# Kernel optimization log

Hardware: AMD Instinct MI355X
Metric: run time of the kernel (lower is better)

## Reference

```python
import jax, jax.numpy as jnp
import numpy as np

B, S, D, V, MAXLEN, K = 1, 2048, 768, 32000, 2048, 3
EPS = 1.1920929e-07  # torch.finfo(float32).eps, nn.RMSNorm default


def _linear_init(key, fan_in, fan_out):
    kw, kb = jax.random.split(key)
    bound = 1.0 / np.sqrt(fan_in)
    w = jax.random.uniform(kw, (fan_in, fan_out), minval=-bound, maxval=bound, dtype=jnp.float32)
    b = jax.random.uniform(kb, (fan_out,), minval=-bound, maxval=bound, dtype=jnp.float32)
    return w, b


def setup_inputs() -> dict:
    key = jax.random.key(0)
    ks = jax.random.split(key, 12)
    x = jax.random.randint(ks[0], (B, S), 0, V, dtype=jnp.int64)
    embedding = jax.random.normal(ks[1], (V, D), dtype=jnp.float32)
    pos_emb = jax.random.normal(ks[2], (MAXLEN, D), dtype=jnp.float32)
    # conv1d weight (out, in, k) torch layout
    bound = 1.0 / np.sqrt(D * K)
    conv_w = jax.random.uniform(ks[3], (D, D, K), minval=-bound, maxval=bound, dtype=jnp.float32)
    conv_b = jax.random.uniform(ks[4], (D,), minval=-bound, maxval=bound, dtype=jnp.float32)
    wg1, bg1 = _linear_init(ks[5], D, D)
    wmv, bmv = _linear_init(ks[6], 2 * D, D)
    wmg, bmg = _linear_init(ks[7], 2 * D, D)
    wrg, brg = _linear_init(ks[8], 2 * D, D)
    whw, bhw = _linear_init(ks[9], D, D)
    rms_w = jnp.ones((D,), dtype=jnp.float32)
    wpred, bpred = _linear_init(ks[10], D, V)
    return dict(x=x, embedding=embedding, pos_emb=pos_emb, conv_w=conv_w, conv_b=conv_b,
                wg1=wg1, bg1=bg1, wmv=wmv, bmv=bmv, wmg=wmg, bmg=bmg,
                wrg=wrg, brg=brg, whw=whw, bhw=bhw, rms_w=rms_w, wpred=wpred, bpred=bpred)


def _rmsnorm(x, w):
    ms = jnp.mean(jnp.square(x), axis=-1, keepdims=True)
    return x * jax.lax.rsqrt(ms + EPS) * w


def _causal_conv(x, conv_w, conv_b):
    # x: [B,S,D] -> left-pad by K-1, conv1d, back to [B,S,D]
    xc = jnp.transpose(x, (0, 2, 1))  # [B,D,S]
    y = jax.lax.conv_general_dilated(
        xc, conv_w, window_strides=(1,), padding=[(K - 1, 0)],
        dimension_numbers=('NCH', 'OIH', 'NCH'))
    y = y + conv_b[None, :, None]
    return jnp.transpose(y, (0, 2, 1))


def reference(x, embedding, pos_emb, conv_w, conv_b, wg1, bg1, wmv, bmv, wmg, bmg,
              wrg, brg, whw, bhw, rms_w, wpred, bpred):
    seq_len = x.shape[1]
    h = embedding[x] + pos_emb[:seq_len][None, :, :]
    h = _causal_conv(h, conv_w, conv_b)
    nodes = h * jax.nn.sigmoid(h @ wg1 + bg1)
    # Hillis-Steele log-depth causal scan
    curr = nodes
    step = 1
    while step < seq_len:
        left = curr[:, :-step, :]
        right = curr[:, step:, :]
        comb = jnp.concatenate([left, right], axis=-1)
        val = comb @ wmv + bmv
        gate = jax.nn.sigmoid(comb @ wmg + bmg)
        merged = _rmsnorm(val * gate, rms_w)
        hg = jax.nn.sigmoid(right @ whw + bhw)
        merged = hg * merged + (1.0 - hg) * right
        rg = jax.nn.sigmoid(comb @ wrg + brg)
        merged = rg * merged + (1.0 - rg) * (left + right) * 0.5
        curr = curr.at[:, step:, :].set(merged)
        step *= 2
    return curr @ wpred + bpred
```

## Files before the change

kernel.cpp:

```cpp
#include <hip/hip_runtime.h>
#include <hip/hip_bf16.h>

typedef __attribute__((ext_vector_type(8))) short short8;
typedef __attribute__((ext_vector_type(4))) float floatx4;
typedef __hip_bfloat16 bf16_t;

#define DD 768

__device__ __forceinline__ float sigmoid_f(float x) { return 1.f / (1.f + __expf(-x)); }

__device__ __forceinline__ void gl2lds16(const void* g, void* l) {
  __builtin_amdgcn_global_load_lds((const __attribute__((address_space(1))) void*)g,
                                   (__attribute__((address_space(3))) void*)l, 16, 0, 0);
}

__global__ __launch_bounds__(512, 2) void gemm256(
    const bf16_t* __restrict__ A, int lda, int M,
    const bf16_t* __restrict__ Wt, int Kdim,
    int nRowT, int nColT,
    const float* __restrict__ bias,
    float* __restrict__ out, int N)
{
  __shared__ __attribute__((aligned(16))) unsigned char lds[163840];
  const int tid = threadIdx.x;
  const int wave = tid >> 6, lane = tid & 63;
  const int l15 = lane & 15, kq = lane >> 4;
  const int wm = wave >> 2, wn = wave & 3;

  const int nwg = gridDim.x;
  const int q8 = nwg >> 3, r8 = nwg & 7;
  const int xcd = blockIdx.x & 7, lin = blockIdx.x >> 3;
  const int wgid = (xcd < r8 ? xcd * (q8 + 1) : r8 * (q8 + 1) + (xcd - r8) * q8) + lin;
  const int rowt = wgid % nRowT, colt = wgid / nRowT;
  const int rowbase = rowt * 256, colbase = colt * 256;

  floatx4 acc[8][4] = {};
  const int nkt = Kdim >> 6;

  auto stageA = [&](int mh, int kt, int buf) {
    const int kbase = kt << 6;
    #pragma unroll
    for (int rr = 0; rr < 2; ++rr) {
      const int L = rr * 64 + wave * 8;
      const int lrow_base = (L >> 6) * 128 + mh * 64 + (L & 63);
      const int lrow = lrow_base + (lane >> 3);
      const int slotp = (lane & 7) ^ (lrow & 7);
      const int gr = min(rowbase + lrow, M - 1);
      gl2lds16(A + (size_t)gr * lda + kbase + slotp * 8,
               lds + buf * 32768 + lrow_base * 128);
    }
  };
  auto stageB = [&](int nh, int kt, int buf) {
    const int kbase = kt << 6;
    #pragma unroll
    for (int rr = 0; rr < 2; ++rr) {
      const int L = rr * 64 + wave * 8;
      const int lrow_base = (L >> 5) * 64 + nh * 32 + (L & 31);
      const int lrow = lrow_base + (lane >> 3);
      const int slotp = (lane & 7) ^ (lrow & 7);
      const int gn = colbase + lrow;
      gl2lds16(Wt + (size_t)gn * Kdim + kbase + slotp * 8,
               lds + 65536 + buf * 32768 + lrow_base * 128);
    }
  };

#define READ_A(av_, mh_) \
  _Pragma("unroll") for (int i = 0; i < 4; ++i) { \
    const int r_ = wm * 128 + (mh_) * 64 + i * 16 + l15; \
    _Pragma("unroll") for (int s = 0; s < 2; ++s) { \
      const int sl_ = (s * 4 + kq) ^ (r_ & 7); \
      av_[i][s] = *reinterpret_cast<const short8*>(Ab + r_ * 128 + sl_ * 16); } }

#define READ_B(bv_, nh_) \
  _Pragma("unroll") for (int j = 0; j < 2; ++j) { \
    const int r_ = wn * 64 + (nh_) * 32 + j * 16 + l15; \
    _Pragma("unroll") for (int s = 0; s < 2; ++s) { \
      const int sl_ = (s * 4 + kq) ^ (r_ & 7); \
      bv_[j][s] = *reinterpret_cast<const short8*>(Bb + r_ * 128 + sl_ * 16); } }

#define MFMA_Q(av_, bv_, mb_, nb_) \
  __builtin_amdgcn_s_setprio(1); \
  _Pragma("unroll") for (int i = 0; i < 4; ++i) \
    _Pragma("unroll") for (int j = 0; j < 2; ++j) \
      _Pragma("unroll") for (int s = 0; s < 2; ++s) \
        acc[(mb_) + i][(nb_) + j] = __builtin_amdgcn_mfma_f32_16x16x32_bf16( \
            av_[i][s], bv_[j][s], acc[(mb_) + i][(nb_) + j], 0, 0, 0); \
  __builtin_amdgcn_s_setprio(0);

  stageB(0, 0, 0); stageB(1, 0, 0);
  stageA(0, 0, 0); stageA(1, 0, 0);
  if (nkt > 1) { stageB(0, 1, 1); stageB(1, 1, 1); }

  short8 av0[4][2], av1[4][2], bv0[2][2], bv1[2][2];
  int curA = 0, curB = 0;
  for (int t = 0; t < nkt; ++t) {
    const bool hasA = (t + 1 < nkt), hasB = (t + 2 < nkt);
    const unsigned char* Ab = lds + curA * 32768;
    const unsigned char* Bb = lds + 65536 + curB * 32768;
    int tgtB = curB + 2; if (tgtB >= 3) tgtB -= 3;

    if (hasA) { asm volatile("s_waitcnt vmcnt(6)" ::: "memory"); }
    else      { asm volatile("s_waitcnt vmcnt(2)" ::: "memory"); }
    __builtin_amdgcn_s_barrier();
    READ_A(av0, 0)
    READ_B(bv0, 0)
    if (hasA) stageA(0, t + 1, curA ^ 1);
    MFMA_Q(av0, bv0, 0, 0)

    READ_B(bv1, 1)
    if (hasA) stageA(1, t + 1, curA ^ 1);
    MFMA_Q(av0, bv1, 0, 2)

    if (hasA) { asm volatile("s_waitcnt vmcnt(8)" ::: "memory"); }
    else      { asm volatile("s_waitcnt vmcnt(0)" ::: "memory"); }
    __builtin_amdgcn_s_barrier();
    READ_A(av1, 1)
    if (hasB) stageB(0, t + 2, tgtB);
    MFMA_Q(av1, bv0, 4, 0)

    if (hasB) stageB(1, t + 2, tgtB);
    MFMA_Q(av1, bv1, 4, 2)

    curA ^= 1; curB = (curB + 1 == 3) ? 0 : curB + 1;
  }
#undef READ_A
#undef READ_B
#undef MFMA_Q

  const int hi = lane >> 4;
  #pragma unroll
  for (int i = 0; i < 8; ++i)
    #pragma unroll
    for (int j = 0; j < 4; ++j) {
      const int c = colbase + wn * 64 + j * 16 + l15;
      const float bb = bias[c];
      #pragma unroll
      for (int rg = 0; rg < 4; ++rg) {
        const int r = rowbase + wm * 128 + i * 16 + hi * 4 + rg;
        if (r < M) out[(size_t)r * N + c] = acc[i][j][rg] + bb;
      }
    }
}

__global__ __launch_bounds__(256, 2) void gemm128(
    const bf16_t* __restrict__ A, int lda, int M, int nRowT,
    int s0, int s1, int s2,
    const bf16_t* __restrict__ Wt, int Kdim,
    const float* __restrict__ bias,
    float* __restrict__ out, int N,
    bf16_t* __restrict__ out_bf,
    const float* __restrict__ gate_other)
{
  __shared__ __attribute__((aligned(16))) unsigned char lds[65536];
  const int tid = threadIdx.x;
  const int wave = tid >> 6, lane = tid & 63;
  const int l15 = lane & 15, kq = lane >> 4;
  const int wm = wave >> 1, wn = wave & 1;

  const int nwg = gridDim.x;
  const int q8 = nwg >> 3, r8 = nwg & 7;
  const int xcd = blockIdx.x & 7, lin = blockIdx.x >> 3;
  const int wgid = (xcd < r8 ? xcd * (q8 + 1) : r8 * (q8 + 1) + (xcd - r8) * q8) + lin;
  const int rowt = wgid % nRowT, colt = wgid / nRowT;
  const int rowbase = rowt * 128, colbase = colt * 128;

  floatx4 acc[4][4] = {};
  const int nkt = Kdim >> 6;

  auto stage = [&](int kt, int buf) {
    const int kbase = kt << 6;
    const int chunk = kbase / 768;
    const int shift = (chunk == 0) ? s0 : ((chunk == 1) ? s1 : s2);
    const int csrc  = kbase - chunk * 768;
    #pragma unroll
    for (int q = 0; q < 4; ++q) {
      const int Lb  = q * 32 + wave * 8;
      const int row = Lb + (lane >> 3);
      const int slotp = (lane & 7) ^ (row & 7);
      const int gr = min(rowbase + row, M - 1) + shift;
      gl2lds16(A + (size_t)gr * lda + csrc + slotp * 8,
               lds + buf * 16384 + Lb * 128);
      const int gn = colbase + row;
      gl2lds16(Wt + (size_t)gn * Kdim + kbase + slotp * 8,
               lds + 32768 + buf * 16384 + Lb * 128);
    }
  };

  stage(0, 0);
  int cur = 0;
  for (int t = 0; t < nkt; ++t) {
    if (t + 1 < nkt) {
      stage(t + 1, cur ^ 1);
      asm volatile("s_waitcnt vmcnt(8)" ::: "memory");
    } else {
      asm volatile("s_waitcnt vmcnt(0)" ::: "memory");
    }
    __builtin_amdgcn_s_barrier();

    const unsigned char* Ab = lds + cur * 16384;
    const unsigned char* Bb = lds + 32768 + cur * 16384;
    short8 av[4][2], bv[4][2];
    #pragma unroll
    for (int i = 0; i < 4; ++i) {
      const int r = wm * 64 + i * 16 + l15;
      #pragma unroll
      for (int s = 0; s < 2; ++s) {
        const int sl = (s * 4 + kq) ^ (r & 7);
        av[i][s] = *reinterpret_cast<const short8*>(Ab + r * 128 + sl * 16);
      }
    }
    #pragma unroll
    for (int j = 0; j < 4; ++j) {
      const int r = wn * 64 + j * 16 + l15;
      #pragma unroll
      for (int s = 0; s < 2; ++s) {
        const int sl = (s * 4 + kq) ^ (r & 7);
        bv[j][s] = *reinterpret_cast<const short8*>(Bb + r * 128 + sl * 16);
      }
    }
    __builtin_amdgcn_s_setprio(1);
    #pragma unroll
    for (int i = 0; i < 4; ++i)
      #pragma unroll
      for (int j = 0; j < 4; ++j)
        #pragma unroll
        for (int s = 0; s < 2; ++s)
          acc[i][j] = __builtin_amdgcn_mfma_f32_16x16x32_bf16(
              av[i][s], bv[j][s], acc[i][j], 0, 0, 0);
    __builtin_amdgcn_s_setprio(0);
    asm volatile("s_waitcnt lgkmcnt(0)" ::: "memory");
    __builtin_amdgcn_s_barrier();
    cur ^= 1;
  }

  const int hi = lane >> 4;
  #pragma unroll
  for (int i = 0; i < 4; ++i)
    #pragma unroll
    for (int j = 0; j < 4; ++j) {
      const int c = colbase + wn * 64 + j * 16 + l15;
      const float bb = bias[c];
      #pragma unroll
      for (int rg = 0; rg < 4; ++rg) {
        const int r = rowbase + wm * 64 + i * 16 + hi * 4 + rg;
        if (r < M) {
          float v = acc[i][j][rg] + bb;
          if (gate_other) v = gate_other[(size_t)r * N + c] * sigmoid_f(v);
          if (out)    out[(size_t)r * N + c] = v;
          if (out_bf) out_bf[(size_t)r * N + c] = __float2bfloat16(v);
        }
      }
    }
}

__global__ void transpose_cvt(const float* __restrict__ in, bf16_t* __restrict__ out,
                              int in_ld, int out_ld)
{
  __shared__ float tile[32][33];
  const int n0 = blockIdx.x * 32, k0 = blockIdx.y * 32;
  const int tx = threadIdx.x, ty = threadIdx.y;
  #pragma unroll
  for (int yy = ty; yy < 32; yy += 8)
    tile[yy][tx] = in[(size_t)(k0 + yy) * in_ld + n0 + tx];
  __syncthreads();
  #pragma unroll
  for (int yy = ty; yy < 32; yy += 8)
    out[(size_t)(n0 + yy) * out_ld + k0 + tx] = __float2bfloat16(tile[tx][yy]);
}

__global__ void build_wct(const float* __restrict__ cw, bf16_t* __restrict__ wct) {
  const int idx = blockIdx.x * 256 + threadIdx.x;
  const int o = idx / 2304, c = idx - o * 2304;
  const int k = c / 768, i = c - k * 768;
  wct[idx] = __float2bfloat16(cw[o * 2304 + i * 3 + k]);
}

__global__ void build_bias(const float* __restrict__ bmv, const float* __restrict__ bmg,
                           const float* __restrict__ brg, const float* __restrict__ bhw,
                           float* __restrict__ out) {
  const int i = blockIdx.x * 256 + threadIdx.x;
  float v;
  if (i < 768) v = bmv[i];
  else if (i < 1536) v = bmg[i - 768];
  else if (i < 2304) v = brg[i - 1536];
  else v = bhw[i - 2304];
  out[i] = v;
}

__global__ void embed_k(const int* __restrict__ x, const float* __restrict__ emb,
                        const float* __restrict__ pos, bf16_t* __restrict__ hpad) {
  const int t = blockIdx.x, tid = threadIdx.x;
  int id = 0, tt = t - 2;
  if (t >= 2) id = x[tt];
  #pragma unroll
  for (int q = 0; q < 3; ++q) {
    const int d = tid + q * 256;
    float v = 0.f;
    if (t >= 2) v = emb[(size_t)id * DD + d] + pos[(size_t)tt * DD + d];
    hpad[(size_t)t * DD + d] = __float2bfloat16(v);
  }
}

__global__ __launch_bounds__(256) void merge_ew(
    const bf16_t* __restrict__ curOldB,
    bf16_t* __restrict__ curNewB,
    const bf16_t* __restrict__ tmp,
    const float* __restrict__ rmsw, int step)
{
  const int t = blockIdx.x, tid = threadIdx.x;
  if (t < step) {
    const uint4* sB = (const uint4*)(curOldB + (size_t)t * DD);
    uint4* dB = (uint4*)(curNewB + (size_t)t * DD);
    if (tid < 96) dB[tid] = sB[tid];
    return;
  }
  const int r = t - step;
  const bf16_t* row = tmp + (size_t)r * 3072;
  float mv[3]; float ss = 0.f;
  #pragma unroll
  for (int q = 0; q < 3; ++q) {
    const int d = tid + q * 256;
    const float m = __bfloat162float(row[d]) * sigmoid_f(__bfloat162float(row[768 + d]));
    mv[q] = m; ss += m * m;
  }
  #pragma unroll
  for (int o = 32; o >= 1; o >>= 1) ss += __shfl_down(ss, o, 64);
  __shared__ float red[4];
  if ((tid & 63) == 0) red[tid >> 6] = ss;
  __syncthreads();
  const float tot = red[0] + red[1] + red[2] + red[3];
  const float scale = rsqrtf(tot * (1.f / 768.f) + 1.1920929e-07f);
  #pragma unroll
  for (int q = 0; q < 3; ++q) {
    const int d = tid + q * 256;
    float merged = mv[q] * scale * rmsw[d];
    const float right = __bfloat162float(curOldB[(size_t)t * DD + d]);
    const float left  = __bfloat162float(curOldB[(size_t)r * DD + d]);
    const float hg = sigmoid_f(__bfloat162float(row[2304 + d]));
    merged = hg * merged + (1.f - hg) * right;
    const float rg = sigmoid_f(__bfloat162float(row[1536 + d]));
    merged = rg * merged + (1.f - rg) * (left + right) * 0.5f;
    curNewB[(size_t)t * DD + d] = __float2bfloat16(merged);
  }
}

extern "C" void kernel_launch(void* const* d_in, const int* in_sizes, int n_in,
                              void* d_out, int out_size, void* d_ws, size_t ws_size,
                              hipStream_t stream) {
  const int*   x      = (const int*)  d_in[0];
  const float* emb    = (const float*)d_in[1];
  const float* pos    = (const float*)d_in[2];
  const float* conv_w = (const float*)d_in[3];
  const float* conv_b = (const float*)d_in[4];
  const float* wg1    = (const float*)d_in[5];
  const float* bg1    = (const float*)d_in[6];
  const float* wmv    = (const float*)d_in[7];
  const float* bmv    = (const float*)d_in[8];
  const float* wmg    = (const float*)d_in[9];
  const float* bmg    = (const float*)d_in[10];
  const float* wrg    = (const float*)d_in[11];
  const float* brg    = (const float*)d_in[12];
  const float* whw    = (const float*)d_in[13];
  const float* bhw    = (const float*)d_in[14];
  const float* rmsw   = (const float*)d_in[15];
  const float* wpred  = (const float*)d_in[16];
  const float* bpred  = (const float*)d_in[17];

  char* ws = (char*)d_ws;
  size_t off = 0;
  auto carve = [&](size_t bytes) { char* p = ws + off; off += (bytes + 255) & ~(size_t)255; return p; };
  bf16_t* wpred_t  = (bf16_t*)carve(32000ull * 768 * 2);
  bf16_t* Wbig_t   = (bf16_t*)carve(3072ull * 1536 * 2);
  bf16_t* wc_t     = (bf16_t*)carve(768ull * 2304 * 2);
  bf16_t* wg1_t    = (bf16_t*)carve(768ull * 768 * 2);
  float*  bias_big = (float*) carve(3072 * 4);
  bf16_t* h_pad    = (bf16_t*)carve(2050ull * 768 * 2);
  float*  hconv    = (float*) carve(2048ull * 768 * 4);
  bf16_t* hconv_bf = (bf16_t*)carve(2048ull * 768 * 2);
  bf16_t* currA_b  = (bf16_t*)carve(2048ull * 768 * 2);
  bf16_t* currB_b  = (bf16_t*)carve(2048ull * 768 * 2);
  bf16_t* tmp_bf   = (bf16_t*)carve(2048ull * 3072 * 2);

  const dim3 tb(32, 8);
  hipMemsetAsync(Wbig_t + 2304ull * 1536, 0, 768ull * 1536 * 2, stream);
  transpose_cvt<<<dim3(24, 48), tb, 0, stream>>>(wmv, Wbig_t,                        768, 1536);
  transpose_cvt<<<dim3(24, 48), tb, 0, stream>>>(wmg, Wbig_t + 768ull * 1536,        768, 1536);
  transpose_cvt<<<dim3(24, 48), tb, 0, stream>>>(wrg, Wbig_t + 1536ull * 1536,       768, 1536);
  transpose_cvt<<<dim3(24, 24), tb, 0, stream>>>(whw, Wbig_t + 2304ull * 1536 + 768, 768, 1536);
  transpose_cvt<<<dim3(24, 24), tb, 0, stream>>>(wg1, wg1_t, 768, 768);
  transpose_cvt<<<dim3(1000, 24), tb, 0, stream>>>(wpred, wpred_t, 32000, 768);
  build_wct<<<6912, 256, 0, stream>>>(conv_w, wc_t);
  build_bias<<<12, 256, 0, stream>>>(bmv, bmg, brg, bhw, bias_big);

  embed_k<<<2050, 256, 0, stream>>>(x, emb, pos, h_pad);

  gemm128<<<16 * 6, 256, 0, stream>>>(h_pad, 768, 2048, 16, 0, 1, 2,
                                      wc_t, 2304, conv_b, hconv, 768, hconv_bf, nullptr);
  gemm128<<<16 * 6, 256, 0, stream>>>(hconv_bf, 768, 2048, 16, 0, 0, 0,
                                      wg1_t, 768, bg1, nullptr, 768, currA_b, hconv);

  bf16_t* curB = currA_b;
  bf16_t* nxtB = currB_b;
  for (int step = 1; step < 2048; step <<= 1) {
    const int M = 2048 - step;
    const int nRowT = (M + 127) / 128;
    gemm128<<<nRowT * 24, 256, 0, stream>>>(
        curB, 768, M, nRowT, 0, step, 0, Wbig_t, 1536, bias_big,
        nullptr, 3072, tmp_bf, nullptr);
    merge_ew<<<2048, 256, 0, stream>>>(curB, nxtB, tmp_bf, rmsw, step);
    { bf16_t* tb_ = curB; curB = nxtB; nxtB = tb_; }
  }

  gemm256<<<8 * 125, 512, 0, stream>>>(curB, 768, 2048, wpred_t, 768, 8, 125,
                                       bpred, (float*)d_out, 32000);
}
```

Measured before the change: 726.2 us.

## Triple-buffer gemm128 with BK=32 tiles and raise occupancy to three blocks

Halves the K-tile depth of the 128x128 GEMM from 64 to 32 and keeps three LDS buffers in rotation, so loads run two tiles ahead with one barrier per iteration instead of two. The LDS footprint drops from 64KB to 48KB, and launch bounds now request three workgroups per CU. The intent is to hide global-to-LDS latency better and raise occupancy. In exchange it doubles the loop iteration count, changes the LDS swizzle, and tightens the register budget per thread.

```diff
diff --git a/kernel.cpp b/kernel.cpp
--- a/kernel.cpp
+++ b/kernel.cpp
@@ -142,7 +142,7 @@
     }
 }
 
-__global__ __launch_bounds__(256, 2) void gemm128(
+__global__ __launch_bounds__(256, 3) void gemm128(
     const bf16_t* __restrict__ A, int lda, int M, int nRowT,
     int s0, int s1, int s2,
     const bf16_t* __restrict__ Wt, int Kdim,
@@ -151,7 +151,7 @@
     bf16_t* __restrict__ out_bf,
     const float* __restrict__ gate_other)
 {
-  __shared__ __attribute__((aligned(16))) unsigned char lds[65536];
+  __shared__ __attribute__((aligned(16))) unsigned char lds[49152];
   const int tid = threadIdx.x;
   const int wave = tid >> 6, lane = tid & 63;
   const int l15 = lane & 15, kq = lane >> 4;
@@ -165,72 +165,67 @@
   const int rowbase = rowt * 128, colbase = colt * 128;
 
   floatx4 acc[4][4] = {};
-  const int nkt = Kdim >> 6;
+  const int nkt = Kdim >> 5;
 
   auto stage = [&](int kt, int buf) {
-    const int kbase = kt << 6;
+    const int kbase = kt << 5;
     const int chunk = kbase / 768;
     const int shift = (chunk == 0) ? s0 : ((chunk == 1) ? s1 : s2);
     const int csrc  = kbase - chunk * 768;
     #pragma unroll
-    for (int q = 0; q < 4; ++q) {
-      const int Lb  = q * 32 + wave * 8;
-      const int row = Lb + (lane >> 3);
-      const int slotp = (lane & 7) ^ (row & 7);
+    for (int rr = 0; rr < 2; ++rr) {
+      const int L = wave * 32 + rr * 16;
+      const int row = L + (lane >> 2);
+      const int sl = (lane & 3) ^ ((row >> 1) & 3);
       const int gr = min(rowbase + row, M - 1) + shift;
-      gl2lds16(A + (size_t)gr * lda + csrc + slotp * 8,
-               lds + buf * 16384 + Lb * 128);
+      gl2lds16(A + (size_t)gr * lda + csrc + sl * 8,
+               lds + buf * 8192 + L * 64);
       const int gn = colbase + row;
-      gl2lds16(Wt + (size_t)gn * Kdim + kbase + slotp * 8,
-               lds + 32768 + buf * 16384 + Lb * 128);
+      gl2lds16(Wt + (size_t)gn * Kdim + kbase + sl * 8,
+               lds + 24576 + buf * 8192 + L * 64);
     }
   };
 
   stage(0, 0);
-  int cur = 0;
+  if (nkt > 1) {
+    stage(1, 1);
+    asm volatile("s_waitcnt vmcnt(4)" ::: "memory");
+  } else {
+    asm volatile("s_waitcnt vmcnt(0)" ::: "memory");
+  }
+  __builtin_amdgcn_s_barrier();
+  __builtin_amdgcn_sched_barrier(0);
+
   for (int t = 0; t < nkt; ++t) {
-    if (t + 1 < nkt) {
-      stage(t + 1, cur ^ 1);
-      asm volatile("s_waitcnt vmcnt(8)" ::: "memory");
-    } else {
-      asm volatile("s_waitcnt vmcnt(0)" ::: "memory");
-    }
-    __builtin_amdgcn_s_barrier();
-
-    const unsigned char* Ab = lds + cur * 16384;
-    const unsigned char* Bb = lds + 32768 + cur * 16384;
-    short8 av[4][2], bv[4][2];
+    if (t + 2 < nkt) { int b = t + 2; while (b >= 3) b -= 3; stage(t + 2, b); }
+    int cb = t; while (cb >= 3) cb -= 3;
+    const unsigned char* Ab = lds + cb * 8192;
+    const unsigned char* Bb = lds + 24576 + cb * 8192;
+    short8 av[4], bv[4];
     #pragma unroll
     for (int i = 0; i < 4; ++i) {
       const int r = wm * 64 + i * 16 + l15;
-      #pragma unroll
-      for (int s = 0; s < 2; ++s) {
-        const int sl = (s * 4 + kq) ^ (r & 7);
-        av[i][s] = *reinterpret_cast<const short8*>(Ab + r * 128 + sl * 16);
-      }
+      av[i] = *reinterpret_cast<const short8*>(Ab + r * 64 + ((kq ^ ((r >> 1) & 3)) << 4));
     }
     #pragma unroll
     for (int j = 0; j < 4; ++j) {
       const int r = wn * 64 + j * 16 + l15;
-      #pragma unroll
-      for (int s = 0; s < 2; ++s) {
-        const int sl = (s * 4 + kq) ^ (r & 7);
-        bv[j][s] = *reinterpret_cast<const short8*>(Bb + r * 128 + sl * 16);
-      }
+      bv[j] = *reinterpret_cast<const short8*>(Bb + r * 64 + ((kq ^ ((r >> 1) & 3)) << 4));
     }
     __builtin_amdgcn_s_setprio(1);
     #pragma unroll
     for (int i = 0; i < 4; ++i)
       #pragma unroll
       for (int j = 0; j < 4; ++j)
-        #pragma unroll
-        for (int s = 0; s < 2; ++s)
-          acc[i][j] = __builtin_amdgcn_mfma_f32_16x16x32_bf16(
-              av[i][s], bv[j][s], acc[i][j], 0, 0, 0);
+        acc[i][j] = __builtin_amdgcn_mfma_f32_16x16x32_bf16(av[i], bv[j], acc[i][j], 0, 0, 0);
     __builtin_amdgcn_s_setprio(0);
-    asm volatile("s_waitcnt lgkmcnt(0)" ::: "memory");
-    __builtin_amdgcn_s_barrier();
-    cur ^= 1;
+    if (t + 1 < nkt) {
+      if (t + 2 < nkt) { asm volatile("s_waitcnt vmcnt(4)" ::: "memory"); }
+      else             { asm volatile("s_waitcnt vmcnt(0)" ::: "memory"); }
+      asm volatile("s_waitcnt lgkmcnt(0)" ::: "memory");
+      __builtin_amdgcn_s_barrier();
+      __builtin_amdgcn_sched_barrier(0);
+    }
   }
 
   const int hi = lane >> 4;
```

Result: slower. 772.0 us (+6.3%).
